# Optimization experiments

Measured on AMD Instinct MI355X. Metric: run time of the kernel, lower is better.

Reference implementation:

```python
import jax, jax.numpy as jnp
import numpy as np

B, NT, D = 256, 301, 96
NSEG = 50


def setup_inputs() -> dict:
    key = jax.random.key(0)
    inp = jax.random.normal(key, (B, NT, D), dtype=jnp.float32)
    return {"inp": inp, "n_segments": NSEG}


def _logsig_depth2(segs):
    # segs: (B, S, L, D) -- per-segment sub-paths (piecewise linear)
    x0 = segs[:, :, :1, :]
    dx = segs[:, :, 1:, :] - segs[:, :, :-1, :]          # increments (B,S,L-1,D)
    xprev = segs[:, :, :-1, :] - x0                      # X(t-) - X(0)
    lvl1 = segs[:, :, -1, :] - segs[:, :, 0, :]          # level-1 logsig (B,S,D)
    # Level-2 signature S_ij = sum_t X_i(t-) dX_j + 0.5 sum_t dX_i dX_j;
    # log-signature level 2 is the antisymmetric part (Levy area), so the
    # symmetric 0.5 dx (x) dx term cancels and we only need M - M^T.
    M = jnp.einsum('bsti,bstj->bsij', xprev, dx)         # (B,S,D,D)
    A = 0.5 * (M - jnp.swapaxes(M, -1, -2))
    iu, ju = np.triu_indices(segs.shape[-1], k=1)
    # words/Lyndon basis at depth 2: coefficients A_ij for i<j, lexicographic
    return jnp.concatenate([lvl1, A[:, :, iu, ju]], axis=-1)


def reference(inp, n_segments):
    # n_segments is a static Python int -> segment index map built at trace time,
    # replicating: t_vec = [round(x) for x in linspace(1, nT, n_segments+1)],
    # segment i = inp[:, t_vec[i]-1 : t_vec[i+1], :]
    nT = inp.shape[1]
    t_vec = [int(round(x)) for x in np.linspace(1, nT, n_segments + 1)]
    idx = np.stack([np.arange(t_vec[i] - 1, t_vec[i + 1]) for i in range(n_segments)])  # (S, L)
    segs = inp[:, idx, :]                                # (B, S, L, D)
    return _logsig_depth2(segs)
```

## Files before the change

### kernel.cpp

```cpp
#include <hip/hip_runtime.h>

#define BB 256
#define NT 301
#define DD 96
#define NSEG 50
#define SEGROWS 7
#define NTRI (DD * (DD - 1) / 2)
#define OUTD (DD + NTRI)

__global__ __launch_bounds__(256)
void logsig_kernel(const float* __restrict__ inp, float* __restrict__ out) {
    const int bs = blockIdx.x;
    const int b  = bs / NSEG;
    const int s  = bs % NSEG;

    __shared__ float seg[SEGROWS * DD];

    const float* src = inp + ((size_t)b * NT + (size_t)6 * s) * DD;
    for (int idx = threadIdx.x; idx < SEGROWS * DD; idx += 256)
        seg[idx] = src[idx];
    __syncthreads();

    float* o = out + (size_t)bs * OUTD;

    if (threadIdx.x < DD)
        o[threadIdx.x] = seg[6 * DD + threadIdx.x] - seg[threadIdx.x];

    const int ty = threadIdx.x >> 4;
    const int tx = threadIdx.x & 15;

    for (int ti = 0; ti < 6; ++ti) {
        const int i = 16 * ti + ty;
        float si[SEGROWS];
        #pragma unroll
        for (int t = 0; t < SEGROWS; ++t) si[t] = seg[t * DD + i];

        for (int tj = ti; tj < 6; ++tj) {
            const int j = 16 * tj + tx;
            if (j > i) {
                float sj[SEGROWS];
                #pragma unroll
                for (int t = 0; t < SEGROWS; ++t) sj[t] = seg[t * DD + j];

                float acc = 0.f;
                #pragma unroll
                for (int t = 1; t < 6; ++t) {
                    const float xpi = si[t] - si[0];
                    const float dxj = sj[t + 1] - sj[t];
                    const float xpj = sj[t] - sj[0];
                    const float dxi = si[t + 1] - si[t];
                    acc += xpi * dxj - xpj * dxi;
                }
                const int tri = i * (2 * DD - 1 - i) / 2 + (j - i - 1);
                o[DD + tri] = 0.5f * acc;
            }
        }
    }
}

extern "C" void kernel_launch(void* const* d_in, const int* in_sizes, int n_in,
                              void* d_out, int out_size, void* d_ws, size_t ws_size,
                              hipStream_t stream) {
    const float* inp = (const float*)d_in[0];
    float* out = (float*)d_out;
    logsig_kernel<<<BB * NSEG, 256, 0, stream>>>(inp, out);
}
```

Before: 294.7 us.

## Precompute path offsets and use linear-combination form with vectorized j-tiles

```diff
diff --git a/kernel.cpp b/kernel.cpp
--- a/kernel.cpp
+++ b/kernel.cpp
@@ -1,12 +1,12 @@
 #include <hip/hip_runtime.h>
 
 #define BB 256
-#define NT 301
+#define NTT 301
 #define DD 96
 #define NSEG 50
-#define SEGROWS 7
 #define NTRI (DD * (DD - 1) / 2)
 #define OUTD (DD + NTRI)
+
 
 __global__ __launch_bounds__(256)
 void logsig_kernel(const float* __restrict__ inp, float* __restrict__ out) {
@@ -14,45 +14,72 @@
     const int b  = bs / NSEG;
     const int s  = bs % NSEG;
 
-    __shared__ float seg[SEGROWS * DD];
+    __shared__ float seg[7 * DD];
+    __shared__ __align__(16) float xs[6 * DD];
 
-    const float* src = inp + ((size_t)b * NT + (size_t)6 * s) * DD;
-    for (int idx = threadIdx.x; idx < SEGROWS * DD; idx += 256)
+    const float* src = inp + ((size_t)b * NTT + (size_t)6 * s) * DD;
+    for (int idx = threadIdx.x; idx < 7 * DD; idx += 256)
         seg[idx] = src[idx];
+    __syncthreads();
+    for (int idx = threadIdx.x; idx < 6 * DD; idx += 256) {
+        const int ch = idx % DD;
+        xs[idx] = seg[idx + DD] - seg[ch];
+    }
     __syncthreads();
 
     float* o = out + (size_t)bs * OUTD;
 
     if (threadIdx.x < DD)
-        o[threadIdx.x] = seg[6 * DD + threadIdx.x] - seg[threadIdx.x];
+        o[threadIdx.x] = xs[5 * DD + threadIdx.x];
 
-    const int ty = threadIdx.x >> 4;
-    const int tx = threadIdx.x & 15;
+    const int ty = threadIdx.x >> 3;
+    const int tx = threadIdx.x & 7;
 
-    for (int ti = 0; ti < 6; ++ti) {
-        const int i = 16 * ti + ty;
-        float si[SEGROWS];
+    #pragma unroll
+    for (int ti = 0; ti < 3; ++ti) {
+        const int i = 32 * ti + ty;
+        const float x1 = xs[0 * DD + i];
+        const float x2 = xs[1 * DD + i];
+        const float x3 = xs[2 * DD + i];
+        const float x4 = xs[3 * DD + i];
+        const float x5 = xs[4 * DD + i];
+        const float x6 = xs[5 * DD + i];
+        const float c1 = -0.5f * x2;
+        const float c2 = 0.5f * (x1 - x3);
+        const float c3 = 0.5f * (x2 - x4);
+        const float c4 = 0.5f * (x3 - x5);
+        const float c5 = 0.5f * (x4 - x6);
+        const float c6 = 0.5f * x5;
+        float* orow = o + DD + i * (2 * DD - 1 - i) / 2 - i - 1;
+
         #pragma unroll
-        for (int t = 0; t < SEGROWS; ++t) si[t] = seg[t * DD + i];
+        for (int tj = ti; tj < 3; ++tj) {
+            const int j0 = 32 * tj + 4 * tx;
+            if (j0 + 3 <= i) continue;
 
-        for (int tj = ti; tj < 6; ++tj) {
-            const int j = 16 * tj + tx;
-            if (j > i) {
-                float sj[SEGROWS];
-                #pragma unroll
-                for (int t = 0; t < SEGROWS; ++t) sj[t] = seg[t * DD + j];
+            float q1[4], q2[4], q3[4], q4[4], q5[4], q6[4];
+            *(float4*)q1 = *(const float4*)&xs[0 * DD + j0];
+            *(float4*)q2 = *(const float4*)&xs[1 * DD + j0];
+            *(float4*)q3 = *(const float4*)&xs[2 * DD + j0];
+            *(float4*)q4 = *(const float4*)&xs[3 * DD + j0];
+            *(float4*)q5 = *(const float4*)&xs[4 * DD + j0];
+            *(float4*)q6 = *(const float4*)&xs[5 * DD + j0];
 
-                float acc = 0.f;
-                #pragma unroll
-                for (int t = 1; t < 6; ++t) {
-                    const float xpi = si[t] - si[0];
-                    const float dxj = sj[t + 1] - sj[t];
-                    const float xpj = sj[t] - sj[0];
-                    const float dxi = si[t + 1] - si[t];
-                    acc += xpi * dxj - xpj * dxi;
-                }
-                const int tri = i * (2 * DD - 1 - i) / 2 + (j - i - 1);
-                o[DD + tri] = 0.5f * acc;
+            float r[4];
+            #pragma unroll
+            for (int e = 0; e < 4; ++e) {
+                float acc = c1 * q1[e];
+                acc = fmaf(c2, q2[e], acc);
+                acc = fmaf(c3, q3[e], acc);
+                acc = fmaf(c4, q4[e], acc);
+                acc = fmaf(c5, q5[e], acc);
+                acc = fmaf(c6, q6[e], acc);
+                r[e] = acc;
+            }
+            #pragma unroll
+            for (int e = 0; e < 4; ++e) {
+                const int j = j0 + e;
+                if (j > i) orow[j] = r[e];
             }
         }
     }
```

Result: slower. 338.4 us (+14.8%).
